# Kernel tuning notes

Measured on AMD Instinct MI355X. Metric: run time of the kernel, lower is better.

Reference implementation:

```python
import jax, jax.numpy as jnp
import numpy as np

NUM_HEADS = 12
D_MODEL = 768
D_HEAD = D_MODEL // NUM_HEADS


def setup_inputs() -> dict:
    key = jax.random.key(0)
    k_x, k_wqkv, k_bqkv, k_wo, k_bo = jax.random.split(key, 5)
    B, S = 1, 4096
    x = jax.random.normal(k_x, (B, S, D_MODEL), dtype=jnp.float32)
    # flax Dense default init: lecun_normal for kernel, zeros for bias
    w_qkv = jax.random.normal(k_wqkv, (D_MODEL, 3 * D_MODEL), dtype=jnp.float32) / np.sqrt(D_MODEL)
    b_qkv = jnp.zeros((3 * D_MODEL,), dtype=jnp.float32)
    w_o = jax.random.normal(k_wo, (D_MODEL, D_MODEL), dtype=jnp.float32) / np.sqrt(D_MODEL)
    b_o = jnp.zeros((D_MODEL,), dtype=jnp.float32)
    return {"x": x, "w_qkv": w_qkv, "b_qkv": b_qkv, "w_o": w_o, "b_o": b_o}


def reference(x, w_qkv, b_qkv, w_o, b_o):
    B, S, _ = x.shape
    H, Dh = NUM_HEADS, D_HEAD
    qkv = jnp.einsum('bsd,de->bse', x, w_qkv) + b_qkv  # [B,S,3*D]
    q, k, v = jnp.split(qkv, 3, axis=-1)
    # [B,S,D] -> [B,H,S,Dh]
    q = q.reshape(B, S, H, Dh).transpose(0, 2, 1, 3)
    k = k.reshape(B, S, H, Dh).transpose(0, 2, 1, 3)
    v = v.reshape(B, S, H, Dh).transpose(0, 2, 1, 3)
    logits = jnp.einsum('bhqd,bhkd->bhqk', q, k) / jnp.sqrt(jnp.float32(Dh))
    weights = jax.nn.softmax(logits, axis=-1)  # deterministic=True -> no dropout
    attn = jnp.einsum('bhqk,bhkd->bhqd', weights, v)
    attn = attn.transpose(0, 2, 1, 3).reshape(B, S, H * Dh)
    return jnp.einsum('bsd,de->bse', attn, w_o) + b_o
```

## Files before the change

kernel.cpp:

```cpp
#include <hip/hip_runtime.h>

typedef unsigned short u16;
typedef __attribute__((ext_vector_type(8))) short bf16x8;
typedef __attribute__((ext_vector_type(4))) float f32x4;

#define CST 0.18033688011112042f

__device__ inline u16 f2bf(float f) {
    unsigned u;
    __builtin_memcpy(&u, &f, 4);
    unsigned r = (u + 0x7FFF + ((u >> 16) & 1)) >> 16;
    return (u16)r;
}
__device__ inline unsigned pack2(float lo, float hi) {
    return (unsigned)f2bf(lo) | ((unsigned)f2bf(hi) << 16);
}
__device__ inline unsigned fbits(float f) {
    unsigned u;
    __builtin_memcpy(&u, &f, 4);
    return u;
}
__device__ inline f32x4 fzero() {
    f32x4 z = {0.f, 0.f, 0.f, 0.f};
    return z;
}
__device__ inline f32x4 mfma16(bf16x8 a, bf16x8 b, f32x4 c) {
    return __builtin_amdgcn_mfma_f32_16x16x32_bf16(a, b, c, 0, 0, 0);
}

__device__ inline void gld_lds16(const u16* g, u16* l) {
    __builtin_amdgcn_global_load_lds(
        reinterpret_cast<const __attribute__((address_space(1))) unsigned int*>(
            reinterpret_cast<uintptr_t>(g)),
        reinterpret_cast<__attribute__((address_space(3))) unsigned int*>(
            static_cast<unsigned int>(reinterpret_cast<uintptr_t>(l))),
        16, 0, 0);
}

#define NB_WQKV (72 * 24)
#define NB_WO   (24 * 24)
#define NB_CVT  (4096 * 768 / 2048)

__global__ __launch_bounds__(256) void prep(const float* __restrict__ x,
                                            const float* __restrict__ w_qkv,
                                            const float* __restrict__ w_o,
                                            u16* __restrict__ xb,
                                            u16* __restrict__ wqkvT,
                                            u16* __restrict__ woT) {
    __shared__ float tile[32][33];
    int bid = blockIdx.x;
    int t = threadIdx.x;
    if (bid < NB_WQKV + NB_WO) {
        const float* in;
        u16* out;
        int bx, by, R, C;
        if (bid < NB_WQKV) {
            in = w_qkv; out = wqkvT; R = 768; C = 2304;
            bx = bid % 72; by = bid / 72;
        } else {
            int b2 = bid - NB_WQKV;
            in = w_o; out = woT; R = 768; C = 768;
            bx = b2 % 24; by = b2 / 24;
        }
        int c0 = bx * 32, r0 = by * 32;
        int tx = t & 31, ty = t >> 5;
#pragma unroll
        for (int j = 0; j < 32; j += 8)
            tile[ty + j][tx] = in[(size_t)(r0 + ty + j) * C + c0 + tx];
        __syncthreads();
#pragma unroll
        for (int j = 0; j < 32; j += 8)
            out[(size_t)(c0 + ty + j) * R + r0 + tx] = f2bf(tile[tx][ty + j]);
    } else {
        int i = (bid - NB_WQKV - NB_WO) * 2048 + t * 8;
        float4 a = *(const float4*)(x + i);
        float4 b = *(const float4*)(x + i + 4);
        uint4 w;
        w.x = pack2(a.x, a.y);
        w.y = pack2(a.z, a.w);
        w.z = pack2(b.x, b.y);
        w.w = pack2(b.z, b.w);
        *(uint4*)(xb + i) = w;
    }
}

__global__ __launch_bounds__(256) void vtrans(const u16* __restrict__ qkv,
                                              u16* __restrict__ vt) {
    __shared__ u16 T[64 * 136];
    int t = threadIdx.x;
    int h = blockIdx.y, kv0 = blockIdx.x * 128;
    {
        int key = t >> 1, ch = (t & 1) * 32;
        const u16* vp = qkv + (size_t)(kv0 + key) * 2304 + 1536 + h * 64 + ch;
        u16 tmp[32];
        *(uint4*)&tmp[0]  = *(const uint4*)vp;
        *(uint4*)&tmp[8]  = *(const uint4*)(vp + 8);
        *(uint4*)&tmp[16] = *(const uint4*)(vp + 16);
        *(uint4*)&tmp[24] = *(const uint4*)(vp + 24);
        int k5 = key & 31, grp = key >> 5;
        int kp = (grp << 5) | (((k5 >> 2) & 3) << 3) | ((k5 >> 4) << 2) | (k5 & 3);
#pragma unroll
        for (int j = 0; j < 32; j++) T[(ch + j) * 136 + kp] = tmp[j];
    }
    __syncthreads();
    {
        int dh = t >> 2, kc = (t & 3) * 32;
        uint4 o0 = *(const uint4*)&T[dh * 136 + kc];
        uint4 o1 = *(const uint4*)&T[dh * 136 + kc + 8];
        uint4 o2 = *(const uint4*)&T[dh * 136 + kc + 16];
        uint4 o3 = *(const uint4*)&T[dh * 136 + kc + 24];
        u16* op = vt + ((size_t)(h * 64 + dh)) * 4096 + kv0 + kc;
        *(uint4*)op = o0;
        *(uint4*)(op + 8) = o1;
        *(uint4*)(op + 16) = o2;
        *(uint4*)(op + 24) = o3;
    }
}

template <int MT, bool OUT_F32, bool SCALE_Q>
__global__ __launch_bounds__(256) void gemm_bt(const u16* __restrict__ A,
                                               const u16* __restrict__ Bt,
                                               const float* __restrict__ bias,
                                               void* __restrict__ Cv,
                                               int M, int N, int K) {
    constexpr int MI = MT / 32;
    constexpr int NA = MT / 64;
    __shared__ u16 As[MT * 32];
    __shared__ u16 Bs[128 * 32];

    int t = threadIdx.x;
    int wave = t >> 6, lane = t & 63, quad = lane >> 4, l16 = lane & 15;
    int mbase = blockIdx.y * MT, nbase = blockIdx.x * 128;
    int mw = (wave & 1) * (MT / 2), nw = (wave >> 1) * 64;

    f32x4 acc[MI][4];
#pragma unroll
    for (int i = 0; i < MI; i++)
#pragma unroll
        for (int j = 0; j < 4; j++) acc[i][j] = fzero();

    int xqs = (lane & 3) ^ ((lane >> 3) & 3);
    const u16* AgL[NA];
    u16* AsL[NA];
#pragma unroll
    for (int j = 0; j < NA; j++) {
        int rl = wave * (MT / 4) + j * 16 + (lane >> 2);
        AgL[j] = A + (size_t)(mbase + rl) * K + xqs * 8;
        AsL[j] = As + wave * (MT / 4) * 32 + j * 512;
    }
    const u16* BgL[2];
    u16* BsL[2];
#pragma unroll
    for (int j = 0; j < 2; j++) {
        int rl = wave * 32 + j * 16 + (lane >> 2);
        BgL[j] = Bt + (size_t)(nbase + rl) * K + xqs * 8;
        BsL[j] = Bs + wave * 1024 + j * 512;
    }

    int xq = quad ^ ((l16 >> 1) & 3);
    int afo[MI], bfo[4];
#pragma unroll
    for (int i = 0; i < MI; i++) afo[i] = (mw + i * 16 + l16) * 32 + xq * 8;
#pragma unroll
    for (int i = 0; i < 4; i++) bfo[i] = (nw + i * 16 + l16) * 32 + xq * 8;

    for (int kt = 0; kt < K; kt += 32) {
#pragma unroll
        for (int j = 0; j < NA; j++) gld_lds16(AgL[j] + kt, AsL[j]);
#pragma unroll
        for (int j = 0; j < 2; j++) gld_lds16(BgL[j] + kt, BsL[j]);
        __syncthreads();

        bf16x8 af[MI], bfr[4];
#pragma unroll
        for (int i = 0; i < MI; i++) af[i] = *(const bf16x8*)&As[afo[i]];
#pragma unroll
        for (int i = 0; i < 4; i++) bfr[i] = *(const bf16x8*)&Bs[bfo[i]];
#pragma unroll
        for (int mi = 0; mi < MI; mi++)
#pragma unroll
            for (int ni = 0; ni < 4; ni++)
                acc[mi][ni] = mfma16(af[mi], bfr[ni], acc[mi][ni]);
        __syncthreads();
    }

#pragma unroll
    for (int ni = 0; ni < 4; ni++) {
        int col = nbase + nw + ni * 16 + l16;
        float bv = bias[col];
        float scale = (SCALE_Q && col < 768) ? CST : 1.0f;
#pragma unroll
        for (int mi = 0; mi < MI; mi++) {
#pragma unroll
            for (int r = 0; r < 4; r++) {
                int row = mbase + mw + mi * 16 + quad * 4 + r;
                float v = (acc[mi][ni][r] + bv) * scale;
                if (OUT_F32)
                    ((float*)Cv)[(size_t)row * N + col] = v;
                else
                    ((u16*)Cv)[(size_t)row * N + col] = f2bf(v);
            }
        }
    }
}

#define SEQ 4096
#define QKV_LD 2304

__global__ __launch_bounds__(256, 2) void attn_flash(const u16* __restrict__ qkv,
                                                     const u16* __restrict__ vt,
                                                     u16* __restrict__ attn) {
    __shared__ __align__(16) char smem[65536];

    int t = threadIdx.x;
    int wave = t >> 6, lane = t & 63, quad = lane >> 4, l16 = lane & 15;
    int h = blockIdx.y;
    int q0 = blockIdx.x * 64;
    const int QOFF = h * 64, KOFF = 768 + h * 64;

    bf16x8 qf[4][2];
#pragma unroll
    for (int qs = 0; qs < 4; qs++) {
        const u16* qp = qkv + (size_t)(q0 + qs * 16 + l16) * QKV_LD + QOFF + quad * 8;
        qf[qs][0] = *(const bf16x8*)(qp);
        qf[qs][1] = *(const bf16x8*)(qp + 32);
    }

    f32x4 o[4][4];
    float l4[4];
#pragma unroll
    for (int qs = 0; qs < 4; qs++) {
        l4[qs] = 0.f;
#pragma unroll
        for (int j = 0; j < 4; j++) o[qs][j] = fzero();
    }

    const u16* kgl[4];
    int kofs[4];
#pragma unroll
    for (int j = 0; j < 4; j++) {
        int r = wave * 32 + j * 8 + (lane >> 3);
        kgl[j] = qkv + (size_t)r * QKV_LD + KOFF +
                 (((lane & 7) ^ ((lane >> 3) & 7)) * 8);
        kofs[j] = (wave * 32 + j * 8) * 64;
    }
    const u16* vgl[4];
    int vofs[4];
#pragma unroll
    for (int j = 0; j < 4; j++) {
        int r = wave * 16 + j * 4 + (lane >> 4);
        vgl[j] = vt + (size_t)(h * 64 + r) * SEQ +
                 (((lane & 15) ^ ((j * 4 + (lane >> 4)) & 7)) * 8);
        vofs[j] = (wave * 16 + j * 4) * 128;
    }

    auto STAGE = [&](int buf, int kv) {
        u16* kb = (u16*)(smem + buf * 16384);
        u16* vb = (u16*)(smem + 32768 + buf * 16384);
#pragma unroll
        for (int j = 0; j < 4; j++) gld_lds16(kgl[j] + (size_t)kv * QKV_LD, kb + kofs[j]);
#pragma unroll
        for (int j = 0; j < 4; j++) gld_lds16(vgl[j] + kv, vb + vofs[j]);
    };

    STAGE(0, 0);
    __syncthreads();

    int cur = 0;
    int x7 = l16 & 7;
    for (int kv0 = 0; kv0 < SEQ; kv0 += 128) {
        if (kv0 + 128 < SEQ) STAGE(cur ^ 1, kv0 + 128);

        const u16* KsB = (const u16*)(smem + cur * 16384);
        const u16* VsB = (const u16*)(smem + 32768 + cur * 16384);

        bf16x8 kf[2][2];
#pragma unroll
        for (int st = 0; st < 2; st++) {
            int r = wave * 32 + st * 16 + l16;
            kf[st][0] = *(const bf16x8*)&KsB[r * 64 + (quad ^ x7) * 8];
            kf[st][1] = *(const bf16x8*)&KsB[r * 64 + ((quad + 4) ^ x7) * 8];
        }
        bf16x8 vf[4];
#pragma unroll
        for (int nt = 0; nt < 4; nt++) {
            int r = nt * 16 + l16;
            vf[nt] = *(const bf16x8*)&VsB[r * 128 + ((wave * 4 + quad) ^ x7) * 8];
        }

        __builtin_amdgcn_s_setprio(1);
#pragma unroll
        for (int qs = 0; qs < 4; qs++) {
            f32x4 s0 = mfma16(kf[0][0], qf[qs][0], fzero());
            s0 = mfma16(kf[0][1], qf[qs][1], s0);
            f32x4 s1 = mfma16(kf[1][0], qf[qs][0], fzero());
            s1 = mfma16(kf[1][1], qf[qs][1], s1);
            float p00 = exp2f(s0[0]), p01 = exp2f(s0[1]);
            float p02 = exp2f(s0[2]), p03 = exp2f(s0[3]);
            float p10 = exp2f(s1[0]), p11 = exp2f(s1[1]);
            float p12 = exp2f(s1[2]), p13 = exp2f(s1[3]);
            l4[qs] += ((p00 + p01) + (p02 + p03)) + ((p10 + p11) + (p12 + p13));
            uint4 pk;
            pk.x = __builtin_amdgcn_perm(fbits(p01), fbits(p00), 0x07060302u);
            pk.y = __builtin_amdgcn_perm(fbits(p03), fbits(p02), 0x07060302u);
            pk.z = __builtin_amdgcn_perm(fbits(p11), fbits(p10), 0x07060302u);
            pk.w = __builtin_amdgcn_perm(fbits(p13), fbits(p12), 0x07060302u);
            bf16x8 pf;
            __builtin_memcpy(&pf, &pk, 16);
#pragma unroll
            for (int nt = 0; nt < 4; nt++)
                o[qs][nt] = mfma16(pf, vf[nt], o[qs][nt]);
        }
        __builtin_amdgcn_s_setprio(0);

        __syncthreads();
        cur ^= 1;
    }

#pragma unroll
    for (int qs = 0; qs < 4; qs++) {
        l4[qs] += __shfl_xor(l4[qs], 16);
        l4[qs] += __shfl_xor(l4[qs], 32);
    }
    float* Lm = (float*)(smem + 34816);
    if (lane < 16) {
#pragma unroll
        for (int qs = 0; qs < 4; qs++) Lm[wave * 64 + qs * 16 + l16] = l4[qs];
    }

    float* M0 = (float*)smem;
    float* M1 = (float*)(smem + 17408);
    __syncthreads();
    if (wave >= 2) {
        float* M = (wave == 2) ? M0 : M1;
#pragma unroll
        for (int qs = 0; qs < 4; qs++)
#pragma unroll
            for (int nt = 0; nt < 4; nt++)
#pragma unroll
                for (int r = 0; r < 4; r++)
                    M[(qs * 16 + quad * 4 + r) * 68 + nt * 16 + l16] = o[qs][nt][r];
    }
    __syncthreads();
    if (wave < 2) {
        float* M = (wave == 0) ? M0 : M1;
#pragma unroll
        for (int qs = 0; qs < 4; qs++)
#pragma unroll
            for (int nt = 0; nt < 4; nt++)
#pragma unroll
                for (int r = 0; r < 4; r++)
                    o[qs][nt][r] += M[(qs * 16 + quad * 4 + r) * 68 + nt * 16 + l16];
    }
    __syncthreads();
    if (wave == 1) {
#pragma unroll
        for (int qs = 0; qs < 4; qs++)
#pragma unroll
            for (int nt = 0; nt < 4; nt++)
#pragma unroll
                for (int r = 0; r < 4; r++)
                    M0[(qs * 16 + quad * 4 + r) * 68 + nt * 16 + l16] = o[qs][nt][r];
    }
    __syncthreads();
    if (wave == 0) {
#pragma unroll
        for (int qs = 0; qs < 4; qs++) {
#pragma unroll
            for (int r = 0; r < 4; r++) {
                int rw = qs * 16 + quad * 4 + r;
                float l = Lm[rw] + Lm[64 + rw] + Lm[128 + rw] + Lm[192 + rw];
                float inv = 1.0f / l;
                u16* op = attn + (size_t)(q0 + rw) * 768 + h * 64;
#pragma unroll
                for (int nt = 0; nt < 4; nt++) {
                    float v = o[qs][nt][r] + M0[rw * 68 + nt * 16 + l16];
                    op[nt * 16 + l16] = f2bf(v * inv);
                }
            }
        }
    }
}

extern "C" void kernel_launch(void* const* d_in, const int* in_sizes, int n_in,
                              void* d_out, int out_size, void* d_ws, size_t ws_size,
                              hipStream_t stream) {
    const float* x      = (const float*)d_in[0];
    const float* w_qkv  = (const float*)d_in[1];
    const float* b_qkv  = (const float*)d_in[2];
    const float* w_o    = (const float*)d_in[3];
    const float* b_o    = (const float*)d_in[4];
    float* out = (float*)d_out;

    u16* wqkvT = (u16*)d_ws;
    u16* woT   = wqkvT + (size_t)2304 * 768;
    u16* qkv   = woT + (size_t)768 * 768;
    u16* attnb = qkv + (size_t)4096 * 2304;
    u16* Vt    = attnb + (size_t)4096 * 768;
    u16* xb    = attnb;

    prep<<<dim3(NB_WQKV + NB_WO + NB_CVT), 256, 0, stream>>>(
        x, w_qkv, w_o, xb, wqkvT, woT);

    gemm_bt<128, false, true><<<dim3(2304 / 128, 4096 / 128), 256, 0, stream>>>(
        xb, wqkvT, b_qkv, qkv, 4096, 2304, 768);

    vtrans<<<dim3(SEQ / 128, 12), 256, 0, stream>>>(qkv, Vt);

    attn_flash<<<dim3(SEQ / 64, 12), 256, 0, stream>>>(qkv, Vt, attnb);

    gemm_bt<64, true, false><<<dim3(768 / 128, 4096 / 64), 256, 0, stream>>>(
        attnb, woT, b_o, out, 4096, 768, 768);
}
```

Baseline: 216.6 us.

## Split attention waves across query and key halves, shrink KV tile for occupancy

Re-partitions the four waves of the flash attention block into a 2x2 grid: each wave now handles 32 query rows and 32 of 64 keys per tile, instead of 64 queries and a quarter of 128 keys. The KV tile drops from 128 to 64 keys, which halves shared memory per block and raises the launch-bounds occupancy target from 2 to 4 blocks. The cross-wave reduction of partial outputs shrinks to a single exchange between two waves instead of a multi-stage four-way reduction. The cost is twice as many loop iterations and barriers, and each K/V fragment is reused across fewer query rows.

```diff
diff --git a/kernel.cpp b/kernel.cpp
--- a/kernel.cpp
+++ b/kernel.cpp
@@ -207,60 +207,61 @@
 #define SEQ 4096
 #define QKV_LD 2304
 
-__global__ __launch_bounds__(256, 2) void attn_flash(const u16* __restrict__ qkv,
+__global__ __launch_bounds__(256, 4) void attn_flash(const u16* __restrict__ qkv,
                                                      const u16* __restrict__ vt,
                                                      u16* __restrict__ attn) {
-    __shared__ __align__(16) char smem[65536];
+    __shared__ __align__(16) char smem[32768];
 
     int t = threadIdx.x;
     int wave = t >> 6, lane = t & 63, quad = lane >> 4, l16 = lane & 15;
+    int kw = wave & 1, qw = wave >> 1;
     int h = blockIdx.y;
     int q0 = blockIdx.x * 64;
     const int QOFF = h * 64, KOFF = 768 + h * 64;
 
-    bf16x8 qf[4][2];
-#pragma unroll
-    for (int qs = 0; qs < 4; qs++) {
-        const u16* qp = qkv + (size_t)(q0 + qs * 16 + l16) * QKV_LD + QOFF + quad * 8;
+    bf16x8 qf[2][2];
+#pragma unroll
+    for (int qs = 0; qs < 2; qs++) {
+        const u16* qp = qkv + (size_t)(q0 + qw * 32 + qs * 16 + l16) * QKV_LD + QOFF + quad * 8;
         qf[qs][0] = *(const bf16x8*)(qp);
         qf[qs][1] = *(const bf16x8*)(qp + 32);
     }
 
-    f32x4 o[4][4];
-    float l4[4];
-#pragma unroll
-    for (int qs = 0; qs < 4; qs++) {
+    f32x4 o[2][4];
+    float l4[2];
+#pragma unroll
+    for (int qs = 0; qs < 2; qs++) {
         l4[qs] = 0.f;
 #pragma unroll
         for (int j = 0; j < 4; j++) o[qs][j] = fzero();
     }
 
-    const u16* kgl[4];
-    int kofs[4];
-#pragma unroll
-    for (int j = 0; j < 4; j++) {
-        int r = wave * 32 + j * 8 + (lane >> 3);
+    const u16* kgl[2];
+    int kofs[2];
+#pragma unroll
+    for (int j = 0; j < 2; j++) {
+        int r = wave * 16 + j * 8 + (lane >> 3);
         kgl[j] = qkv + (size_t)r * QKV_LD + KOFF +
                  (((lane & 7) ^ ((lane >> 3) & 7)) * 8);
-        kofs[j] = (wave * 32 + j * 8) * 64;
-    }
-    const u16* vgl[4];
-    int vofs[4];
-#pragma unroll
-    for (int j = 0; j < 4; j++) {
-        int r = wave * 16 + j * 4 + (lane >> 4);
+        kofs[j] = (wave * 16 + j * 8) * 64;
+    }
+    const u16* vgl[2];
+    int vofs[2];
+#pragma unroll
+    for (int j = 0; j < 2; j++) {
+        int r = wave * 16 + j * 8 + (lane >> 3);
         vgl[j] = vt + (size_t)(h * 64 + r) * SEQ +
-                 (((lane & 15) ^ ((j * 4 + (lane >> 4)) & 7)) * 8);
-        vofs[j] = (wave * 16 + j * 4) * 128;
+                 (((lane & 7) ^ ((lane >> 3) & 7)) * 8);
+        vofs[j] = (wave * 16 + j * 8) * 64;
     }
 
     auto STAGE = [&](int buf, int kv) {
-        u16* kb = (u16*)(smem + buf * 16384);
-        u16* vb = (u16*)(smem + 32768 + buf * 16384);
-#pragma unroll
-        for (int j = 0; j < 4; j++) gld_lds16(kgl[j] + (size_t)kv * QKV_LD, kb + kofs[j]);
-#pragma unroll
-        for (int j = 0; j < 4; j++) gld_lds16(vgl[j] + kv, vb + vofs[j]);
+        u16* kb = (u16*)(smem + buf * 8192);
+        u16* vb = (u16*)(smem + 16384 + buf * 8192);
+#pragma unroll
+        for (int j = 0; j < 2; j++) gld_lds16(kgl[j] + (size_t)kv * QKV_LD, kb + kofs[j]);
+#pragma unroll
+        for (int j = 0; j < 2; j++) gld_lds16(vgl[j] + kv, vb + vofs[j]);
     };
 
     STAGE(0, 0);
@@ -268,16 +269,16 @@
 
     int cur = 0;
     int x7 = l16 & 7;
-    for (int kv0 = 0; kv0 < SEQ; kv0 += 128) {
-        if (kv0 + 128 < SEQ) STAGE(cur ^ 1, kv0 + 128);
-
-        const u16* KsB = (const u16*)(smem + cur * 16384);
-        const u16* VsB = (const u16*)(smem + 32768 + cur * 16384);
+    for (int kv0 = 0; kv0 < SEQ; kv0 += 64) {
+        if (kv0 + 64 < SEQ) STAGE(cur ^ 1, kv0 + 64);
+
+        const u16* KsB = (const u16*)(smem + cur * 8192);
+        const u16* VsB = (const u16*)(smem + 16384 + cur * 8192);
 
         bf16x8 kf[2][2];
 #pragma unroll
         for (int st = 0; st < 2; st++) {
-            int r = wave * 32 + st * 16 + l16;
+            int r = kw * 32 + st * 16 + l16;
             kf[st][0] = *(const bf16x8*)&KsB[r * 64 + (quad ^ x7) * 8];
             kf[st][1] = *(const bf16x8*)&KsB[r * 64 + ((quad + 4) ^ x7) * 8];
         }
@@ -285,12 +286,12 @@
 #pragma unroll
         for (int nt = 0; nt < 4; nt++) {
             int r = nt * 16 + l16;
-            vf[nt] = *(const bf16x8*)&VsB[r * 128 + ((wave * 4 + quad) ^ x7) * 8];
+            vf[nt] = *(const bf16x8*)&VsB[r * 64 + ((kw * 4 + quad) ^ x7) * 8];
         }
 
         __builtin_amdgcn_s_setprio(1);
 #pragma unroll
-        for (int qs = 0; qs < 4; qs++) {
+        for (int qs = 0; qs < 2; qs++) {
             f32x4 s0 = mfma16(kf[0][0], qf[qs][0], fzero());
             s0 = mfma16(kf[0][1], qf[qs][1], s0);
             f32x4 s1 = mfma16(kf[1][0], qf[qs][0], fzero());
@@ -318,65 +319,54 @@
     }
 
 #pragma unroll
-    for (int qs = 0; qs < 4; qs++) {
+    for (int qs = 0; qs < 2; qs++) {
         l4[qs] += __shfl_xor(l4[qs], 16);
         l4[qs] += __shfl_xor(l4[qs], 32);
     }
-    float* Lm = (float*)(smem + 34816);
+    float* M0 = (float*)smem;
+    float* Lm = (float*)(smem + 17408);
     if (lane < 16) {
-#pragma unroll
-        for (int qs = 0; qs < 4; qs++) Lm[wave * 64 + qs * 16 + l16] = l4[qs];
-    }
-
-    float* M0 = (float*)smem;
-    float* M1 = (float*)(smem + 17408);
+        Lm[kw * 64 + qw * 32 + l16] = l4[0];
+        Lm[kw * 64 + qw * 32 + 16 + l16] = l4[1];
+    }
+    if (kw == 1) {
+#pragma unroll
+        for (int nt = 0; nt < 4; nt++)
+#pragma unroll
+            for (int r = 0; r < 4; r++)
+                M0[(qw * 32 + quad * 4 + r) * 68 + nt * 16 + l16] = o[0][nt][r];
+    } else {
+#pragma unroll
+        for (int nt = 0; nt < 4; nt++)
+#pragma unroll
+            for (int r = 0; r < 4; r++)
+                M0[(qw * 32 + 16 + quad * 4 + r) * 68 + nt * 16 + l16] = o[1][nt][r];
+    }
     __syncthreads();
-    if (wave >= 2) {
-        float* M = (wave == 2) ? M0 : M1;
-#pragma unroll
-        for (int qs = 0; qs < 4; qs++)
-#pragma unroll
-            for (int nt = 0; nt < 4; nt++)
-#pragma unroll
-                for (int r = 0; r < 4; r++)
-                    M[(qs * 16 + quad * 4 + r) * 68 + nt * 16 + l16] = o[qs][nt][r];
-    }
-    __syncthreads();
-    if (wave < 2) {
-        float* M = (wave == 0) ? M0 : M1;
-#pragma unroll
-        for (int qs = 0; qs < 4; qs++)
-#pragma unroll
-            for (int nt = 0; nt < 4; nt++)
-#pragma unroll
-                for (int r = 0; r < 4; r++)
-                    o[qs][nt][r] += M[(qs * 16 + quad * 4 + r) * 68 + nt * 16 + l16];
-    }
-    __syncthreads();
-    if (wave == 1) {
-#pragma unroll
-        for (int qs = 0; qs < 4; qs++)
-#pragma unroll
-            for (int nt = 0; nt < 4; nt++)
-#pragma unroll
-                for (int r = 0; r < 4; r++)
-                    M0[(qs * 16 + quad * 4 + r) * 68 + nt * 16 + l16] = o[qs][nt][r];
-    }
-    __syncthreads();
-    if (wave == 0) {
-#pragma unroll
-        for (int qs = 0; qs < 4; qs++) {
-#pragma unroll
-            for (int r = 0; r < 4; r++) {
-                int rw = qs * 16 + quad * 4 + r;
-                float l = Lm[rw] + Lm[64 + rw] + Lm[128 + rw] + Lm[192 + rw];
-                float inv = 1.0f / l;
-                u16* op = attn + (size_t)(q0 + rw) * 768 + h * 64;
-#pragma unroll
-                for (int nt = 0; nt < 4; nt++) {
-                    float v = o[qs][nt][r] + M0[rw * 68 + nt * 16 + l16];
-                    op[nt * 16 + l16] = f2bf(v * inv);
-                }
+    if (kw == 0) {
+#pragma unroll
+        for (int r = 0; r < 4; r++) {
+            int rw = qw * 32 + quad * 4 + r;
+            float l = Lm[rw] + Lm[64 + rw];
+            float inv = 1.0f / l;
+            u16* op = attn + (size_t)(q0 + rw) * 768 + h * 64;
+#pragma unroll
+            for (int nt = 0; nt < 4; nt++) {
+                float v = o[0][nt][r] + M0[rw * 68 + nt * 16 + l16];
+                op[nt * 16 + l16] = f2bf(v * inv);
+            }
+        }
+    } else {
+#pragma unroll
+        for (int r = 0; r < 4; r++) {
+            int rw = qw * 32 + 16 + quad * 4 + r;
+            float l = Lm[rw] + Lm[64 + rw];
+            float inv = 1.0f / l;
+            u16* op = attn + (size_t)(q0 + rw) * 768 + h * 64;
+#pragma unroll
+            for (int nt = 0; nt < 4; nt++) {
+                float v = o[1][nt][r] + M0[rw * 68 + nt * 16 + l16];
+                op[nt * 16 + l16] = f2bf(v * inv);
             }
         }
     }
```

Measured after the change: 201.0 us. -7.2%, faster.
